# Kernel optimization log

Hardware: AMD Instinct MI355X
Metric: run time of the kernel (lower is better)

## Reference

```python
import jax, jax.numpy as jnp
import numpy as np

N, K, D = 131072, 2048, 512


def setup_inputs() -> dict:
    key = jax.random.key(0)
    kx, kc = jax.random.split(key)
    x = jax.random.normal(kx, (N, D), dtype=jnp.float32)
    cluster_centers = jax.random.normal(kc, (K, D), dtype=jnp.float32)
    return {"x": x, "cluster_centers": cluster_centers}


def reference(x, cluster_centers):
    # d_{nk} = ||x_n - c_k||_2; argmin over k.
    x2 = jnp.sum(x * x, axis=-1, keepdims=True)            # [N,1]
    c2 = jnp.sum(cluster_centers * cluster_centers, -1)    # [K]
    d2 = x2 + c2 - 2.0 * (x @ cluster_centers.T)           # [N,K]
    # sqrt is monotonic, so argmin over squared distances equals argmin over L2 norms
    return jnp.argmin(d2, axis=-1)                          # [N] int
```

## Files before the change

kernel.cpp:

```cpp
#include <hip/hip_runtime.h>


#define N_PTS 131072
#define K_CL  2048
#define D_DIM 512
#define BM 128
#define BN 128
#define BK 32

typedef _Float16 half8  __attribute__((ext_vector_type(8)));
typedef _Float16 half4v __attribute__((ext_vector_type(4)));
typedef float    floatx4 __attribute__((ext_vector_type(4)));

#define GLL(g, l) __builtin_amdgcn_global_load_lds( \
    (__attribute__((address_space(1))) void*)(g),   \
    (__attribute__((address_space(3))) void*)(l), 16, 0, 0)

__global__ void row_norms_kernel(const float* __restrict__ A,
                                 float* __restrict__ out, int rows) {
    int gid  = blockIdx.x * blockDim.x + threadIdx.x;
    int wave = gid >> 6;
    int lane = gid & 63;
    if (wave >= rows) return;
    const float4* a = (const float4*)(A + (size_t)wave * D_DIM);
    float4 p = a[lane];
    float4 q = a[lane + 64];
    float s = p.x*p.x + p.y*p.y + p.z*p.z + p.w*p.w
            + q.x*q.x + q.y*q.y + q.z*q.z + q.w*q.w;
    #pragma unroll
    for (int off = 32; off > 0; off >>= 1) s += __shfl_down(s, off, 64);
    if (lane == 0) out[wave] = s;
}

__global__ void conv_f16x2_kernel(const float* __restrict__ src,
                                  _Float16* __restrict__ hi,
                                  _Float16* __restrict__ lo, int n4) {
    int i = blockIdx.x * blockDim.x + threadIdx.x;
    if (i >= n4) return;
    float4 v = ((const float4*)src)[i];
    half4v h, l;
    h.x = (_Float16)v.x; h.y = (_Float16)v.y;
    h.z = (_Float16)v.z; h.w = (_Float16)v.w;
    l.x = (_Float16)(v.x - (float)h.x);
    l.y = (_Float16)(v.y - (float)h.y);
    l.z = (_Float16)(v.z - (float)h.z);
    l.w = (_Float16)(v.w - (float)h.w);
    *(half4v*)(hi + (size_t)i * 4) = h;
    *(half4v*)(lo + (size_t)i * 4) = l;
}

template<bool XPRE, bool CPRE>
__global__ __launch_bounds__(256, 3)
void kmeans_mfma(const float* __restrict__ X, const float* __restrict__ C,
                 const _Float16* __restrict__ Xhi, const _Float16* __restrict__ Xlo,
                 const _Float16* __restrict__ Chi, const _Float16* __restrict__ Clo,
                 const float* __restrict__ c2g, int* __restrict__ out) {
    __shared__ __align__(16) _Float16 sXh[BM * BK], sXl[BM * BK];
    __shared__ __align__(16) _Float16 sCh[BN * BK], sCl[BN * BK];
    __shared__ float c2s[K_CL];
    __shared__ float x2s[BM];

    const int tid  = threadIdx.x;
    const int lane = tid & 63;
    const int w    = tid >> 6;
    const int wti  = w >> 1;
    const int wtj  = w & 1;
    const int q    = lane >> 4;
    const int m16  = lane & 15;
    const int rowBase = blockIdx.x * BM;

    if (CPRE) {
        for (int i = tid; i < K_CL / 4; i += 256)
            ((float4*)c2s)[i] = ((const float4*)c2g)[i];
    } else {
        for (int k = tid; k < K_CL; k += 256) {
            const float4* cp = (const float4*)(C + (size_t)k * D_DIM);
            float s0 = 0.f, s1 = 0.f;
            for (int j = 0; j < D_DIM / 4; j += 2) {
                float4 a = cp[j], b = cp[j + 1];
                s0 += a.x*a.x + a.y*a.y + a.z*a.z + a.w*a.w;
                s1 += b.x*b.x + b.y*b.y + b.z*b.z + b.w*b.w;
            }
            c2s[k] = s0 + s1;
        }
    }
    {
        int r = tid & 127, h = tid >> 7;
        const float4* xp = (const float4*)(X + (size_t)(rowBase + r) * D_DIM + h * 256);
        float s0 = 0.f, s1 = 0.f;
        for (int j = 0; j < 64; j += 2) {
            float4 a = xp[j], b = xp[j + 1];
            s0 += a.x*a.x + a.y*a.y + a.z*a.z + a.w*a.w;
            s1 += b.x*b.x + b.y*b.y + b.z*b.z + b.w*b.w;
        }
        ((float*)sXh)[tid] = s0 + s1;
    }
    __syncthreads();
    if (tid < BM) x2s[tid] = ((float*)sXh)[tid] + ((float*)sXh)[tid + 128];

    float bestV[4][4];
    int   bestI[4][4];
    #pragma unroll
    for (int ti = 0; ti < 4; ++ti)
        #pragma unroll
        for (int r = 0; r < 4; ++r) { bestV[ti][r] = 3.4e38f; bestI[ti][r] = 0; }

    const int s_c4 = tid & 7;
    const int s_r0 = tid >> 3;

    #pragma unroll 1
    for (int kt = 0; kt < K_CL / BN; ++kt) {
        const int k0 = kt * BN;
        floatx4 acc[4][4];
        #pragma unroll
        for (int ti = 0; ti < 4; ++ti)
            #pragma unroll
            for (int tj = 0; tj < 4; ++tj) acc[ti][tj] = (floatx4){0.f, 0.f, 0.f, 0.f};

        #pragma unroll 1
        for (int dt = 0; dt < D_DIM / BK; ++dt) {
            const int d0 = dt * BK;
            __syncthreads();
            if (XPRE) {
                #pragma unroll
                for (int s = 0; s < 2; ++s) {
                    int c = w * 2 + s;
                    int r = c * 16 + (lane >> 2);
                    size_t go = (size_t)(rowBase + r) * D_DIM + d0 + (lane & 3) * 8;
                    GLL(Xhi + go, &sXh[c * 512]);
                    GLL(Xlo + go, &sXl[c * 512]);
                }
            } else {
                #pragma unroll
                for (int p = 0; p < 4; ++p) {
                    int r = s_r0 + p * 32;
                    float4 v = *(const float4*)&X[(size_t)(rowBase + r) * D_DIM + d0 + s_c4 * 4];
                    half4v h, l;
                    h.x = (_Float16)v.x; h.y = (_Float16)v.y;
                    h.z = (_Float16)v.z; h.w = (_Float16)v.w;
                    l.x = (_Float16)(v.x - (float)h.x);
                    l.y = (_Float16)(v.y - (float)h.y);
                    l.z = (_Float16)(v.z - (float)h.z);
                    l.w = (_Float16)(v.w - (float)h.w);
                    *(half4v*)&sXh[r * BK + s_c4 * 4] = h;
                    *(half4v*)&sXl[r * BK + s_c4 * 4] = l;
                }
            }
            if (CPRE) {
                #pragma unroll
                for (int s = 0; s < 2; ++s) {
                    int c = w * 2 + s;
                    int r = c * 16 + (lane >> 2);
                    size_t go = (size_t)(k0 + r) * D_DIM + d0 + (lane & 3) * 8;
                    GLL(Chi + go, &sCh[c * 512]);
                    GLL(Clo + go, &sCl[c * 512]);
                }
            } else {
                #pragma unroll
                for (int p = 0; p < 4; ++p) {
                    int r = s_r0 + p * 32;
                    float4 v = *(const float4*)&C[(size_t)(k0 + r) * D_DIM + d0 + s_c4 * 4];
                    half4v h, l;
                    h.x = (_Float16)v.x; h.y = (_Float16)v.y;
                    h.z = (_Float16)v.z; h.w = (_Float16)v.w;
                    l.x = (_Float16)(v.x - (float)h.x);
                    l.y = (_Float16)(v.y - (float)h.y);
                    l.z = (_Float16)(v.z - (float)h.z);
                    l.w = (_Float16)(v.w - (float)h.w);
                    *(half4v*)&sCh[r * BK + s_c4 * 4] = h;
                    *(half4v*)&sCl[r * BK + s_c4 * 4] = l;
                }
            }
            __syncthreads();

            half8 ah[4], al[4];
            #pragma unroll
            for (int ti = 0; ti < 4; ++ti) {
                int row = wti * 64 + ti * 16 + m16;
                ah[ti] = *(const half8*)&sXh[row * BK + q * 8];
                al[ti] = *(const half8*)&sXl[row * BK + q * 8];
            }
            #pragma unroll
            for (int tj = 0; tj < 4; ++tj) {
                int col = wtj * 64 + tj * 16 + m16;
                half8 bh = *(const half8*)&sCh[col * BK + q * 8];
                half8 bl = *(const half8*)&sCl[col * BK + q * 8];
                #pragma unroll
                for (int ti = 0; ti < 4; ++ti) {
                    floatx4 a = acc[ti][tj];
                    a = __builtin_amdgcn_mfma_f32_16x16x32_f16(ah[ti], bh, a, 0, 0, 0);
                    a = __builtin_amdgcn_mfma_f32_16x16x32_f16(ah[ti], bl, a, 0, 0, 0);
                    a = __builtin_amdgcn_mfma_f32_16x16x32_f16(al[ti], bh, a, 0, 0, 0);
                    acc[ti][tj] = a;
                }
            }
        }

        #pragma unroll
        for (int tj = 0; tj < 4; ++tj) {
            int col = k0 + wtj * 64 + tj * 16 + m16;
            float cv = c2s[col];
            #pragma unroll
            for (int ti = 0; ti < 4; ++ti)
                #pragma unroll
                for (int r = 0; r < 4; ++r) {
                    float s = x2s[wti * 64 + ti * 16 + q * 4 + r] + cv;
                    float v = s - 2.0f * acc[ti][tj][r];
                    if (v < bestV[ti][r]) { bestV[ti][r] = v; bestI[ti][r] = col; }
                }
        }
    }

    #pragma unroll
    for (int ti = 0; ti < 4; ++ti)
        #pragma unroll
        for (int r = 0; r < 4; ++r) {
            float v = bestV[ti][r]; int ix = bestI[ti][r];
            #pragma unroll
            for (int off = 1; off < 16; off <<= 1) {
                float ov = __shfl_xor(v, off, 64);
                int   oi = __shfl_xor(ix, off, 64);
                if (ov < v || (ov == v && oi < ix)) { v = ov; ix = oi; }
            }
            bestV[ti][r] = v; bestI[ti][r] = ix;
        }

    __syncthreads();
    float* rv  = (float*)sXh;
    int*   rix = (int*)sCh;
    if (m16 == 0) {
        #pragma unroll
        for (int ti = 0; ti < 4; ++ti)
            #pragma unroll
            for (int r = 0; r < 4; ++r) {
                int rloc = wti * 64 + ti * 16 + q * 4 + r;
                rv[rloc * 2 + wtj]  = bestV[ti][r];
                rix[rloc * 2 + wtj] = bestI[ti][r];
            }
    }
    __syncthreads();
    if (tid < BM) {
        float v0 = rv[tid * 2], v1 = rv[tid * 2 + 1];
        int   i0 = rix[tid * 2], i1 = rix[tid * 2 + 1];
        out[rowBase + tid] = (v1 < v0 || (v1 == v0 && i1 < i0)) ? i1 : i0;
    }
}

extern "C" void kernel_launch(void* const* d_in, const int* in_sizes, int n_in,
                              void* d_out, int out_size, void* d_ws, size_t ws_size,
                              hipStream_t stream) {
    const float* X = (const float*)d_in[0];
    const float* C = (const float*)d_in[1];
    int* out = (int*)d_out;

    char* ws = (char*)d_ws;
    const size_t c2_off  = 0;
    const size_t chi_off = (size_t)K_CL * 4;
    const size_t clo_off = chi_off + (size_t)K_CL * D_DIM * 2;
    const size_t xhi_off = clo_off + (size_t)K_CL * D_DIM * 2;
    const size_t xlo_off = xhi_off + (size_t)N_PTS * D_DIM * 2;
    const size_t need_C    = xhi_off;
    const size_t need_full = xlo_off + (size_t)N_PTS * D_DIM * 2;

    if (ws_size >= need_full) {
        float*    c2  = (float*)(ws + c2_off);
        _Float16* Chi = (_Float16*)(ws + chi_off);
        _Float16* Clo = (_Float16*)(ws + clo_off);
        _Float16* Xhi = (_Float16*)(ws + xhi_off);
        _Float16* Xlo = (_Float16*)(ws + xlo_off);
        row_norms_kernel<<<(K_CL * 64) / 256, 256, 0, stream>>>(C, c2, K_CL);
        conv_f16x2_kernel<<<(K_CL * D_DIM / 4) / 256, 256, 0, stream>>>(
            C, Chi, Clo, K_CL * D_DIM / 4);
        conv_f16x2_kernel<<<(N_PTS * D_DIM / 4 + 255) / 256, 256, 0, stream>>>(
            X, Xhi, Xlo, N_PTS * D_DIM / 4);
        kmeans_mfma<true, true><<<N_PTS / BM, 256, 0, stream>>>(
            X, C, Xhi, Xlo, Chi, Clo, c2, out);
    } else if (ws_size >= need_C) {
        float*    c2  = (float*)(ws + c2_off);
        _Float16* Chi = (_Float16*)(ws + chi_off);
        _Float16* Clo = (_Float16*)(ws + clo_off);
        row_norms_kernel<<<(K_CL * 64) / 256, 256, 0, stream>>>(C, c2, K_CL);
        conv_f16x2_kernel<<<(K_CL * D_DIM / 4) / 256, 256, 0, stream>>>(
            C, Chi, Clo, K_CL * D_DIM / 4);
        kmeans_mfma<false, true><<<N_PTS / BM, 256, 0, stream>>>(
            X, C, nullptr, nullptr, Chi, Clo, c2, out);
    } else {
        kmeans_mfma<false, false><<<N_PTS / BM, 256, 0, stream>>>(
            X, C, nullptr, nullptr, nullptr, nullptr, nullptr, out);
    }
}
```

Measured before the change: 1.338 ms.

## Double-buffer LDS tiles with prefetch, XOR-swizzle layout, and MFMA priority

Splits the shared-memory tiles into two buffers and flattens the K/D tile loops into one stream, so the next tile's global-to-LDS load is issued before computing on the current one. This cuts a barrier per step and overlaps memory latency with MFMA work. It also XOR-swizzles the LDS column offsets to avoid bank conflicts on the half8 reads, and raises wave priority around the MFMA block. The doubled LDS footprint forces lowering launch bounds from 3 to 2 blocks per CU, which reduces occupancy.

```diff
diff --git a/kernel.cpp b/kernel.cpp
--- a/kernel.cpp
+++ b/kernel.cpp
@@ -7,6 +7,9 @@
 #define BM 128
 #define BN 128
 #define BK 32
+#define NKT (K_CL / BN)
+#define NDT (D_DIM / BK)
+#define NT  (NKT * NDT)
 
 typedef _Float16 half8  __attribute__((ext_vector_type(8)));
 typedef _Float16 half4v __attribute__((ext_vector_type(4)));
@@ -50,13 +53,13 @@
 }
 
 template<bool XPRE, bool CPRE>
-__global__ __launch_bounds__(256, 3)
+__global__ __launch_bounds__(256, 2)
 void kmeans_mfma(const float* __restrict__ X, const float* __restrict__ C,
                  const _Float16* __restrict__ Xhi, const _Float16* __restrict__ Xlo,
                  const _Float16* __restrict__ Chi, const _Float16* __restrict__ Clo,
                  const float* __restrict__ c2g, int* __restrict__ out) {
-    __shared__ __align__(16) _Float16 sXh[BM * BK], sXl[BM * BK];
-    __shared__ __align__(16) _Float16 sCh[BN * BK], sCl[BN * BK];
+    __shared__ __align__(16) _Float16 sXh[2][BM * BK], sXl[2][BM * BK];
+    __shared__ __align__(16) _Float16 sCh[2][BN * BK], sCl[2][BN * BK];
     __shared__ float c2s[K_CL];
     __shared__ float x2s[BM];
 
@@ -68,6 +71,9 @@
     const int q    = lane >> 4;
     const int m16  = lane & 15;
     const int rowBase = blockIdx.x * BM;
+
+    const int jsrc = (((lane & 3) ^ ((lane >> 3) & 3)) * 8);
+    const int swq8 = ((q ^ ((m16 >> 1) & 3)) * 8);
 
     if (CPRE) {
         for (int i = tid; i < K_CL / 4; i += 256)
@@ -97,6 +103,72 @@
     }
     __syncthreads();
     if (tid < BM) x2s[tid] = ((float*)sXh)[tid] + ((float*)sXh)[tid + 128];
+    __syncthreads();
+
+    const int s_c4 = tid & 7;
+    const int s_r0 = tid >> 3;
+
+    auto stage = [&](int t) {
+        const int dtl = t & (NDT - 1);
+        const int ktl = t >> 4;
+        const int d0  = dtl * BK;
+        const int k0l = ktl * BN;
+        const int b   = t & 1;
+        _Float16* dXh = sXh[b]; _Float16* dXl = sXl[b];
+        _Float16* dCh = sCh[b]; _Float16* dCl = sCl[b];
+        if constexpr (XPRE) {
+            #pragma unroll
+            for (int s = 0; s < 2; ++s) {
+                const int cc = w * 2 + s;
+                const int r  = cc * 16 + (lane >> 2);
+                const size_t go = (size_t)(rowBase + r) * D_DIM + d0 + jsrc;
+                GLL(Xhi + go, &dXh[cc * 512]);
+                GLL(Xlo + go, &dXl[cc * 512]);
+            }
+        } else {
+            #pragma unroll
+            for (int p = 0; p < 4; ++p) {
+                const int r = s_r0 + p * 32;
+                float4 v = *(const float4*)&X[(size_t)(rowBase + r) * D_DIM + d0 + s_c4 * 4];
+                half4v h, l;
+                h.x = (_Float16)v.x; h.y = (_Float16)v.y;
+                h.z = (_Float16)v.z; h.w = (_Float16)v.w;
+                l.x = (_Float16)(v.x - (float)h.x);
+                l.y = (_Float16)(v.y - (float)h.y);
+                l.z = (_Float16)(v.z - (float)h.z);
+                l.w = (_Float16)(v.w - (float)h.w);
+                const int off = r * BK + (((s_c4 >> 1) ^ ((r >> 1) & 3)) * 8) + (s_c4 & 1) * 4;
+                *(half4v*)&dXh[off] = h;
+                *(half4v*)&dXl[off] = l;
+            }
+        }
+        if constexpr (CPRE) {
+            #pragma unroll
+            for (int s = 0; s < 2; ++s) {
+                const int cc = w * 2 + s;
+                const int r  = cc * 16 + (lane >> 2);
+                const size_t go = (size_t)(k0l + r) * D_DIM + d0 + jsrc;
+                GLL(Chi + go, &dCh[cc * 512]);
+                GLL(Clo + go, &dCl[cc * 512]);
+            }
+        } else {
+            #pragma unroll
+            for (int p = 0; p < 4; ++p) {
+                const int r = s_r0 + p * 32;
+                float4 v = *(const float4*)&C[(size_t)(k0l + r) * D_DIM + d0 + s_c4 * 4];
+                half4v h, l;
+                h.x = (_Float16)v.x; h.y = (_Float16)v.y;
+                h.z = (_Float16)v.z; h.w = (_Float16)v.w;
+                l.x = (_Float16)(v.x - (float)h.x);
+                l.y = (_Float16)(v.y - (float)h.y);
+                l.z = (_Float16)(v.z - (float)h.z);
+                l.w = (_Float16)(v.w - (float)h.w);
+                const int off = r * BK + (((s_c4 >> 1) ^ ((r >> 1) & 3)) * 8) + (s_c4 & 1) * 4;
+                *(half4v*)&dCh[off] = h;
+                *(half4v*)&dCl[off] = l;
+            }
+        }
+    };
 
     float bestV[4][4];
     int   bestI[4][4];
@@ -105,11 +177,11 @@
         #pragma unroll
         for (int r = 0; r < 4; ++r) { bestV[ti][r] = 3.4e38f; bestI[ti][r] = 0; }
 
-    const int s_c4 = tid & 7;
-    const int s_r0 = tid >> 3;
+    stage(0);
+    __syncthreads();
 
     #pragma unroll 1
-    for (int kt = 0; kt < K_CL / BN; ++kt) {
+    for (int kt = 0; kt < NKT; ++kt) {
         const int k0 = kt * BN;
         floatx4 acc[4][4];
         #pragma unroll
@@ -117,74 +189,28 @@
             #pragma unroll
             for (int tj = 0; tj < 4; ++tj) acc[ti][tj] = (floatx4){0.f, 0.f, 0.f, 0.f};
 
-        #pragma unroll 1
-        for (int dt = 0; dt < D_DIM / BK; ++dt) {
-            const int d0 = dt * BK;
-            __syncthreads();
-            if (XPRE) {
-                #pragma unroll
-                for (int s = 0; s < 2; ++s) {
-                    int c = w * 2 + s;
-                    int r = c * 16 + (lane >> 2);
-                    size_t go = (size_t)(rowBase + r) * D_DIM + d0 + (lane & 3) * 8;
-                    GLL(Xhi + go, &sXh[c * 512]);
-                    GLL(Xlo + go, &sXl[c * 512]);
-                }
-            } else {
-                #pragma unroll
-                for (int p = 0; p < 4; ++p) {
-                    int r = s_r0 + p * 32;
-                    float4 v = *(const float4*)&X[(size_t)(rowBase + r) * D_DIM + d0 + s_c4 * 4];
-                    half4v h, l;
-                    h.x = (_Float16)v.x; h.y = (_Float16)v.y;
-                    h.z = (_Float16)v.z; h.w = (_Float16)v.w;
-                    l.x = (_Float16)(v.x - (float)h.x);
-                    l.y = (_Float16)(v.y - (float)h.y);
-                    l.z = (_Float16)(v.z - (float)h.z);
-                    l.w = (_Float16)(v.w - (float)h.w);
-                    *(half4v*)&sXh[r * BK + s_c4 * 4] = h;
-                    *(half4v*)&sXl[r * BK + s_c4 * 4] = l;
-                }
-            }
-            if (CPRE) {
-                #pragma unroll
-                for (int s = 0; s < 2; ++s) {
-                    int c = w * 2 + s;
-                    int r = c * 16 + (lane >> 2);
-                    size_t go = (size_t)(k0 + r) * D_DIM + d0 + (lane & 3) * 8;
-                    GLL(Chi + go, &sCh[c * 512]);
-                    GLL(Clo + go, &sCl[c * 512]);
-                }
-            } else {
-                #pragma unroll
-                for (int p = 0; p < 4; ++p) {
-                    int r = s_r0 + p * 32;
-                    float4 v = *(const float4*)&C[(size_t)(k0 + r) * D_DIM + d0 + s_c4 * 4];
-                    half4v h, l;
-                    h.x = (_Float16)v.x; h.y = (_Float16)v.y;
-                    h.z = (_Float16)v.z; h.w = (_Float16)v.w;
-                    l.x = (_Float16)(v.x - (float)h.x);
-                    l.y = (_Float16)(v.y - (float)h.y);
-                    l.z = (_Float16)(v.z - (float)h.z);
-                    l.w = (_Float16)(v.w - (float)h.w);
-                    *(half4v*)&sCh[r * BK + s_c4 * 4] = h;
-                    *(half4v*)&sCl[r * BK + s_c4 * 4] = l;
-                }
-            }
-            __syncthreads();
+        #pragma unroll 2
+        for (int dt = 0; dt < NDT; ++dt) {
+            const int t = kt * NDT + dt;
+            if (t + 1 < NT) stage(t + 1);
+
+            const int b = t & 1;
+            const _Float16* bXh = sXh[b]; const _Float16* bXl = sXl[b];
+            const _Float16* bCh = sCh[b]; const _Float16* bCl = sCl[b];
 
             half8 ah[4], al[4];
             #pragma unroll
             for (int ti = 0; ti < 4; ++ti) {
-                int row = wti * 64 + ti * 16 + m16;
-                ah[ti] = *(const half8*)&sXh[row * BK + q * 8];
-                al[ti] = *(const half8*)&sXl[row * BK + q * 8];
-            }
+                const int row = wti * 64 + ti * 16 + m16;
+                ah[ti] = *(const half8*)&bXh[row * BK + swq8];
+                al[ti] = *(const half8*)&bXl[row * BK + swq8];
+            }
+            __builtin_amdgcn_s_setprio(1);
             #pragma unroll
             for (int tj = 0; tj < 4; ++tj) {
-                int col = wtj * 64 + tj * 16 + m16;
-                half8 bh = *(const half8*)&sCh[col * BK + q * 8];
-                half8 bl = *(const half8*)&sCl[col * BK + q * 8];
+                const int col = wtj * 64 + tj * 16 + m16;
+                half8 bh = *(const half8*)&bCh[col * BK + swq8];
+                half8 bl = *(const half8*)&bCl[col * BK + swq8];
                 #pragma unroll
                 for (int ti = 0; ti < 4; ++ti) {
                     floatx4 a = acc[ti][tj];
@@ -194,6 +220,8 @@
                     acc[ti][tj] = a;
                 }
             }
+            __builtin_amdgcn_s_setprio(0);
+            __syncthreads();
         }
 
         #pragma unroll
```

Measured after the change: 1.277 ms. 4.6% less time.

## Load MFMA fragments directly from global into registers with double buffering

Applied to the files above, without the earlier changes.

Removes the LDS staging of X/C tiles and the per-step block barriers. Each wave now loads its MFMA operand fragments straight from global (or L2) into a two-slot register buffer, prefetching the next step while the current one computes, and raises MFMA priority with s_setprio. Occupancy is lowered to two blocks per CU to make room for the larger register footprint. The trade-off is that operands are no longer shared through LDS, so each wave issues its own global loads for data other waves also use, which adds cache and memory traffic.

```diff
diff --git a/kernel.cpp b/kernel.cpp
--- a/kernel.cpp
+++ b/kernel.cpp
@@ -7,14 +7,13 @@
 #define BM 128
 #define BN 128
 #define BK 32
+#define NKT (K_CL / BN)
+#define NDT (D_DIM / BK)
+#define NT  (NKT * NDT)
 
 typedef _Float16 half8  __attribute__((ext_vector_type(8)));
 typedef _Float16 half4v __attribute__((ext_vector_type(4)));
 typedef float    floatx4 __attribute__((ext_vector_type(4)));
-
-#define GLL(g, l) __builtin_amdgcn_global_load_lds( \
-    (__attribute__((address_space(1))) void*)(g),   \
-    (__attribute__((address_space(3))) void*)(l), 16, 0, 0)
 
 __global__ void row_norms_kernel(const float* __restrict__ A,
                                  float* __restrict__ out, int rows) {
@@ -49,16 +48,28 @@
     *(half4v*)(lo + (size_t)i * 4) = l;
 }
 
+#define CVT8(H_, L_, U_, V_) do {                                   \
+    half8 h_, l_;                                                   \
+    h_[0] = (_Float16)(U_).x; l_[0] = (_Float16)((U_).x - (float)h_[0]); \
+    h_[1] = (_Float16)(U_).y; l_[1] = (_Float16)((U_).y - (float)h_[1]); \
+    h_[2] = (_Float16)(U_).z; l_[2] = (_Float16)((U_).z - (float)h_[2]); \
+    h_[3] = (_Float16)(U_).w; l_[3] = (_Float16)((U_).w - (float)h_[3]); \
+    h_[4] = (_Float16)(V_).x; l_[4] = (_Float16)((V_).x - (float)h_[4]); \
+    h_[5] = (_Float16)(V_).y; l_[5] = (_Float16)((V_).y - (float)h_[5]); \
+    h_[6] = (_Float16)(V_).z; l_[6] = (_Float16)((V_).z - (float)h_[6]); \
+    h_[7] = (_Float16)(V_).w; l_[7] = (_Float16)((V_).w - (float)h_[7]); \
+    (H_) = h_; (L_) = l_;                                           \
+} while (0)
+
 template<bool XPRE, bool CPRE>
-__global__ __launch_bounds__(256, 3)
+__global__ __launch_bounds__(256, 2)
 void kmeans_mfma(const float* __restrict__ X, const float* __restrict__ C,
                  const _Float16* __restrict__ Xhi, const _Float16* __restrict__ Xlo,
                  const _Float16* __restrict__ Chi, const _Float16* __restrict__ Clo,
                  const float* __restrict__ c2g, int* __restrict__ out) {
-    __shared__ __align__(16) _Float16 sXh[BM * BK], sXl[BM * BK];
-    __shared__ __align__(16) _Float16 sCh[BN * BK], sCl[BN * BK];
     __shared__ float c2s[K_CL];
     __shared__ float x2s[BM];
+    __shared__ float sred[256];
 
     const int tid  = threadIdx.x;
     const int lane = tid & 63;
@@ -93,10 +104,65 @@
             s0 += a.x*a.x + a.y*a.y + a.z*a.z + a.w*a.w;
             s1 += b.x*b.x + b.y*b.y + b.z*b.z + b.w*b.w;
         }
-        ((float*)sXh)[tid] = s0 + s1;
-    }
-    __syncthreads();
-    if (tid < BM) x2s[tid] = ((float*)sXh)[tid] + ((float*)sXh)[tid + 128];
+        sred[tid] = s0 + s1;
+    }
+    __syncthreads();
+    if (tid < BM) x2s[tid] = sred[tid] + sred[tid + 128];
+    __syncthreads();
+
+    const uint32_t aoffBase = (uint32_t)(rowBase + wti * 64 + m16) * D_DIM + q * 8;
+    const uint32_t boffBase = (uint32_t)(wtj * 64 + m16) * D_DIM + q * 8;
+
+    half8 fah[2][4], fal[2][4], fbh[2][4], fbl[2][4];
+    floatx4 acc[4][4];
+
+    #define LOADF(S_, T_) do {                                             \
+        const int t_   = (T_);                                             \
+        const int dtl_ = t_ & (NDT - 1);                                   \
+        const int ktl_ = t_ >> 4;                                          \
+        const uint32_t ao_ = aoffBase + (uint32_t)dtl_ * BK;               \
+        const uint32_t bo_ = boffBase + (uint32_t)(ktl_ * BN) * D_DIM      \
+                                      + (uint32_t)dtl_ * BK;               \
+        _Pragma("unroll")                                                  \
+        for (int ti_ = 0; ti_ < 4; ++ti_) {                                \
+            const uint32_t o_ = ao_ + ti_ * 16 * D_DIM;                    \
+            if constexpr (XPRE) {                                          \
+                fah[S_][ti_] = *(const half8*)&Xhi[o_];                    \
+                fal[S_][ti_] = *(const half8*)&Xlo[o_];                    \
+            } else {                                                       \
+                float4 u_ = *(const float4*)&X[o_];                        \
+                float4 v_ = *(const float4*)&X[o_ + 4];                    \
+                CVT8(fah[S_][ti_], fal[S_][ti_], u_, v_);                  \
+            }                                                              \
+        }                                                                  \
+        _Pragma("unroll")                                                  \
+        for (int tj_ = 0; tj_ < 4; ++tj_) {                                \
+            const uint32_t o_ = bo_ + tj_ * 16 * D_DIM;                    \
+            if constexpr (CPRE) {                                          \
+                fbh[S_][tj_] = *(const half8*)&Chi[o_];                    \
+                fbl[S_][tj_] = *(const half8*)&Clo[o_];                    \
+            } else {                                                       \
+                float4 u_ = *(const float4*)&C[o_];                        \
+                float4 v_ = *(const float4*)&C[o_ + 4];                    \
+                CVT8(fbh[S_][tj_], fbl[S_][tj_], u_, v_);                  \
+            }                                                              \
+        }                                                                  \
+    } while (0)
+
+    #define MFMA48(S_) do {                                                \
+        __builtin_amdgcn_s_setprio(1);                                     \
+        _Pragma("unroll")                                                  \
+        for (int tj_ = 0; tj_ < 4; ++tj_)                                  \
+            _Pragma("unroll")                                              \
+            for (int ti_ = 0; ti_ < 4; ++ti_) {                            \
+                floatx4 a_ = acc[ti_][tj_];                                \
+                a_ = __builtin_amdgcn_mfma_f32_16x16x32_f16(fah[S_][ti_], fbh[S_][tj_], a_, 0, 0, 0); \
+                a_ = __builtin_amdgcn_mfma_f32_16x16x32_f16(fah[S_][ti_], fbl[S_][tj_], a_, 0, 0, 0); \
+                a_ = __builtin_amdgcn_mfma_f32_16x16x32_f16(fal[S_][ti_], fbh[S_][tj_], a_, 0, 0, 0); \
+                acc[ti_][tj_] = a_;                                        \
+            }                                                              \
+        __builtin_amdgcn_s_setprio(0);                                     \
+    } while (0)
 
     float bestV[4][4];
     int   bestI[4][4];
@@ -105,95 +171,23 @@
         #pragma unroll
         for (int r = 0; r < 4; ++r) { bestV[ti][r] = 3.4e38f; bestI[ti][r] = 0; }
 
-    const int s_c4 = tid & 7;
-    const int s_r0 = tid >> 3;
+    LOADF(0, 0);
 
     #pragma unroll 1
-    for (int kt = 0; kt < K_CL / BN; ++kt) {
+    for (int kt = 0; kt < NKT; ++kt) {
         const int k0 = kt * BN;
-        floatx4 acc[4][4];
         #pragma unroll
         for (int ti = 0; ti < 4; ++ti)
             #pragma unroll
             for (int tj = 0; tj < 4; ++tj) acc[ti][tj] = (floatx4){0.f, 0.f, 0.f, 0.f};
 
         #pragma unroll 1
-        for (int dt = 0; dt < D_DIM / BK; ++dt) {
-            const int d0 = dt * BK;
-            __syncthreads();
-            if (XPRE) {
-                #pragma unroll
-                for (int s = 0; s < 2; ++s) {
-                    int c = w * 2 + s;
-                    int r = c * 16 + (lane >> 2);
-                    size_t go = (size_t)(rowBase + r) * D_DIM + d0 + (lane & 3) * 8;
-                    GLL(Xhi + go, &sXh[c * 512]);
-                    GLL(Xlo + go, &sXl[c * 512]);
-                }
-            } else {
-                #pragma unroll
-                for (int p = 0; p < 4; ++p) {
-                    int r = s_r0 + p * 32;
-                    float4 v = *(const float4*)&X[(size_t)(rowBase + r) * D_DIM + d0 + s_c4 * 4];
-                    half4v h, l;
-                    h.x = (_Float16)v.x; h.y = (_Float16)v.y;
-                    h.z = (_Float16)v.z; h.w = (_Float16)v.w;
-                    l.x = (_Float16)(v.x - (float)h.x);
-                    l.y = (_Float16)(v.y - (float)h.y);
-                    l.z = (_Float16)(v.z - (float)h.z);
-                    l.w = (_Float16)(v.w - (float)h.w);
-                    *(half4v*)&sXh[r * BK + s_c4 * 4] = h;
-                    *(half4v*)&sXl[r * BK + s_c4 * 4] = l;
-                }
-            }
-            if (CPRE) {
-                #pragma unroll
-                for (int s = 0; s < 2; ++s) {
-                    int c = w * 2 + s;
-                    int r = c * 16 + (lane >> 2);
-                    size_t go = (size_t)(k0 + r) * D_DIM + d0 + (lane & 3) * 8;
-                    GLL(Chi + go, &sCh[c * 512]);
-                    GLL(Clo + go, &sCl[c * 512]);
-                }
-            } else {
-                #pragma unroll
-                for (int p = 0; p < 4; ++p) {
-                    int r = s_r0 + p * 32;
-                    float4 v = *(const float4*)&C[(size_t)(k0 + r) * D_DIM + d0 + s_c4 * 4];
-                    half4v h, l;
-                    h.x = (_Float16)v.x; h.y = (_Float16)v.y;
-                    h.z = (_Float16)v.z; h.w = (_Float16)v.w;
-                    l.x = (_Float16)(v.x - (float)h.x);
-                    l.y = (_Float16)(v.y - (float)h.y);
-                    l.z = (_Float16)(v.z - (float)h.z);
-                    l.w = (_Float16)(v.w - (float)h.w);
-                    *(half4v*)&sCh[r * BK + s_c4 * 4] = h;
-                    *(half4v*)&sCl[r * BK + s_c4 * 4] = l;
-                }
-            }
-            __syncthreads();
-
-            half8 ah[4], al[4];
-            #pragma unroll
-            for (int ti = 0; ti < 4; ++ti) {
-                int row = wti * 64 + ti * 16 + m16;
-                ah[ti] = *(const half8*)&sXh[row * BK + q * 8];
-                al[ti] = *(const half8*)&sXl[row * BK + q * 8];
-            }
-            #pragma unroll
-            for (int tj = 0; tj < 4; ++tj) {
-                int col = wtj * 64 + tj * 16 + m16;
-                half8 bh = *(const half8*)&sCh[col * BK + q * 8];
-                half8 bl = *(const half8*)&sCl[col * BK + q * 8];
-                #pragma unroll
-                for (int ti = 0; ti < 4; ++ti) {
-                    floatx4 a = acc[ti][tj];
-                    a = __builtin_amdgcn_mfma_f32_16x16x32_f16(ah[ti], bh, a, 0, 0, 0);
-                    a = __builtin_amdgcn_mfma_f32_16x16x32_f16(ah[ti], bl, a, 0, 0, 0);
-                    a = __builtin_amdgcn_mfma_f32_16x16x32_f16(al[ti], bh, a, 0, 0, 0);
-                    acc[ti][tj] = a;
-                }
-            }
+        for (int dt = 0; dt < NDT; dt += 2) {
+            const int t = kt * NDT + dt;
+            if (t + 1 < NT) LOADF(1, t + 1);
+            MFMA48(0);
+            if (t + 2 < NT) LOADF(0, t + 2);
+            MFMA48(1);
         }
 
         #pragma unroll
@@ -210,6 +204,8 @@
                 }
         }
     }
+    #undef MFMA48
+    #undef LOADF
 
     #pragma unroll
     for (int ti = 0; ti < 4; ++ti)
@@ -226,8 +222,8 @@
         }
 
     __syncthreads();
-    float* rv  = (float*)sXh;
-    int*   rix = (int*)sCh;
+    float* rv  = c2s;
+    int*   rix = (int*)(c2s + 1024);
     if (m16 == 0) {
         #pragma unroll
         for (int ti = 0; ti < 4; ++ti)
```

Result: slower. 2.249 ms (+68.1%).
